# Performance work log

Hardware: AMD Instinct MI355X
Metric: run time of the kernel (lower is better)

Reference implementation:

```python
import jax, jax.numpy as jnp
import numpy as np

DIM = 1024
HEADS = 16
HEAD_DIM = DIM // HEADS

def setup_inputs() -> dict:
    key = jax.random.key(0)
    ks = jax.random.split(key, 5)
    x = jax.random.normal(ks[0], (4, 2048, DIM), dtype=jnp.float32)
    s = DIM ** -0.5
    W_qkv = jax.random.normal(ks[1], (DIM, 3 * DIM), dtype=jnp.float32) * s
    b_qkv = jnp.zeros((3 * DIM,), dtype=jnp.float32)
    W_proj = jax.random.normal(ks[2], (DIM, DIM), dtype=jnp.float32) * s
    b_proj = jnp.zeros((DIM,), dtype=jnp.float32)
    return {"x": x, "W_qkv": W_qkv, "b_qkv": b_qkv, "W_proj": W_proj, "b_proj": b_proj}

def reference(x, W_qkv, b_qkv, W_proj, b_proj):
    B, S, D = x.shape
    scale = HEAD_DIM ** -0.5
    qkv = x @ W_qkv + b_qkv                      # [B,S,3D]
    q, k, v = jnp.split(qkv, 3, axis=-1)         # each [B,S,D]
    def heads(t):
        return t.reshape(B, S, HEADS, HEAD_DIM).transpose(0, 2, 1, 3)  # [B,H,S,d]
    q, k, v = heads(q), heads(k), heads(v)
    attn = jnp.einsum('bhqd,bhkd->bhqk', q, k) * scale
    attn = jax.nn.softmax(attn, axis=-1)
    out = jnp.einsum('bhqk,bhkd->bhqd', attn, v)  # [B,H,S,d]
    out = out.transpose(0, 2, 1, 3).reshape(B, S, D)
    return out @ W_proj + b_proj
```

## Files before the change

kernel.cpp:

```cpp
#include <hip/hip_runtime.h>
#include <hip/hip_bf16.h>
#include <cstdint>


#define SEQ   2048
#define NDIM  1024
#define HEADS 16
#define HD    64

typedef __attribute__((ext_vector_type(8))) short bf16x8;
typedef __attribute__((ext_vector_type(4))) float f32x4;

typedef __attribute__((address_space(1))) void glob_void;
typedef __attribute__((address_space(3))) void lds_void;

__device__ __forceinline__ float b2f(short s) {
    return __uint_as_float(((uint32_t)(uint16_t)s) << 16);
}
__device__ __forceinline__ short f2b(float f) {
    uint32_t u = __float_as_uint(f);
    u += 0x7FFF + ((u >> 16) & 1);
    return (short)(u >> 16);
}
__device__ __forceinline__ uint32_t pk2(float a, float b) {
    return (uint32_t)(uint16_t)f2b(a) | ((uint32_t)(uint16_t)f2b(b) << 16);
}

__global__ __launch_bounds__(256) void sentinel_k(float* __restrict__ out, float v, int n) {
    const int i = blockIdx.x * 256 + threadIdx.x;
    if (i < n) out[i] = v;
}

__global__ __launch_bounds__(256) void transpose_k(const float* __restrict__ W,
                                                   short* __restrict__ WT,
                                                   int R, int C) {
    __shared__ short t[32][33];
    const int bx = blockIdx.x * 32;
    const int by = blockIdx.y * 32;
    const int tx = threadIdx.x, ty = threadIdx.y;
#pragma unroll
    for (int i = 0; i < 32; i += 8)
        t[ty + i][tx] = f2b(W[(size_t)(by + ty + i) * C + bx + tx]);
    __syncthreads();
#pragma unroll
    for (int i = 0; i < 32; i += 8)
        WT[(size_t)(bx + ty + i) * R + by + tx] = t[tx][ty + i];
}

__global__ __launch_bounds__(256) void gemm_bt(const void* __restrict__ A,
                                               const short* __restrict__ BT,
                                               const float* __restrict__ bias,
                                               void* __restrict__ Cout,
                                               int N, int K, int lda,
                                               int amode, int cmode) {
    __shared__ short As[128 * 64];
    __shared__ short Bs[128 * 64];

    const short* Ab = (const short*)A;
    const float* Af = (const float*)A;

    const int tid  = threadIdx.x;
    const int lane = tid & 63;
    const int wid  = tid >> 6;
    const int ln16 = lane & 15;
    const int quad = lane >> 4;
    const int wm = (wid & 1) * 64;
    const int wn = (wid >> 1) * 64;
    const int bm = blockIdx.y * 128;
    const int bn = blockIdx.x * 128;

    f32x4 acc[4][4];
#pragma unroll
    for (int i = 0; i < 4; ++i)
#pragma unroll
        for (int j = 0; j < 4; ++j) {
            acc[i][j][0] = 0.f; acc[i][j][1] = 0.f; acc[i][j][2] = 0.f; acc[i][j][3] = 0.f;
        }

    const int rbase = tid >> 3;
    const int k8    = (tid & 7) * 8;

    for (int ks = 0; ks < K; ks += 64) {
        __syncthreads();
#pragma unroll
        for (int i = 0; i < 4; ++i) {
            const int row = i * 32 + rbase;
            const int c   = i * 256 + tid;
            const short* gb = BT + (size_t)(bn + row) * K + ks + k8;
            __builtin_amdgcn_global_load_lds((glob_void*)gb, (lds_void*)(Bs + c * 8), 16, 0, 0);
        }
        if (amode) {
#pragma unroll
            for (int i = 0; i < 4; ++i) {
                const int row = i * 32 + rbase;
                const int c   = i * 256 + tid;
                const short* ga = Ab + (size_t)(bm + row) * lda + ks + k8;
                __builtin_amdgcn_global_load_lds((glob_void*)ga, (lds_void*)(As + c * 8), 16, 0, 0);
            }
        } else {
#pragma unroll
            for (int i = 0; i < 4; ++i) {
                const int row = i * 32 + rbase;
                const int c   = i * 256 + tid;
                const float* ga = Af + (size_t)(bm + row) * lda + ks + k8;
                const float4 f0 = *(const float4*)ga;
                const float4 f1 = *(const float4*)(ga + 4);
                union { bf16x8 v; short s[8]; } u;
                u.s[0] = f2b(f0.x); u.s[1] = f2b(f0.y); u.s[2] = f2b(f0.z); u.s[3] = f2b(f0.w);
                u.s[4] = f2b(f1.x); u.s[5] = f2b(f1.y); u.s[6] = f2b(f1.z); u.s[7] = f2b(f1.w);
                *(bf16x8*)(As + c * 8) = u.v;
            }
        }
        __syncthreads();

#pragma unroll
        for (int kk = 0; kk < 2; ++kk) {
            bf16x8 a[4], b[4];
#pragma unroll
            for (int t = 0; t < 4; ++t) {
                a[t] = *(const bf16x8*)(As + (wm + t * 16 + ln16) * 64 + kk * 32 + quad * 8);
                b[t] = *(const bf16x8*)(Bs + (wn + t * 16 + ln16) * 64 + kk * 32 + quad * 8);
            }
#pragma unroll
            for (int tm = 0; tm < 4; ++tm)
#pragma unroll
                for (int tn = 0; tn < 4; ++tn)
                    acc[tm][tn] = __builtin_amdgcn_mfma_f32_16x16x32_bf16(a[tm], b[tn], acc[tm][tn], 0, 0, 0);
        }
    }

#pragma unroll
    for (int tm = 0; tm < 4; ++tm) {
        const int row = bm + wm + tm * 16 + quad * 4;
#pragma unroll
        for (int tn = 0; tn < 4; ++tn) {
            const int col = bn + wn + tn * 16 + ln16;
            const float bv = bias[col];
#pragma unroll
            for (int r = 0; r < 4; ++r) {
                const float cv = acc[tm][tn][r] + bv;
                const size_t idx = (size_t)(row + r) * N + col;
                if (cmode) ((float*)Cout)[idx] = cv;
                else       ((short*)Cout)[idx] = f2b(cv);
            }
        }
    }
}

__global__ __launch_bounds__(256, 3) void attn_k(short* qkv) {
    __shared__ __attribute__((aligned(16))) char smem[51200];
    short*    Ks   = (short*)smem;
    uint32_t* VTw  = (uint32_t*)(smem + 16384);
    short*    Ps   = (short*)(smem + 33792);
    float*    Obuf = (float*)smem;
    float*    lred = (float*)(smem + 33792);

    const int tid  = threadIdx.x;
    const int lane = tid & 63;
    const int wid  = tid >> 6;
    const int ln16 = lane & 15;
    const int quad = lane >> 4;

    const int bx = blockIdx.x;
    const int qt = bx & 31;
    const int bh = bx >> 5;
    const int b  = bh >> 4;
    const int h  = bh & 15;
    const int q0 = qt * 64;

    const size_t row0 = ((size_t)b * SEQ) * 3072 + h * HD;

#pragma unroll
    for (int i = 0; i < 2; ++i) {
        const int c = i * 256 + tid;
        __builtin_amdgcn_global_load_lds(
            (glob_void*)(qkv + row0 + (size_t)(q0 + (c >> 3)) * 3072 + (c & 7) * 8),
            (lds_void*)(Ps + c * 8), 16, 0, 0);
    }
    __syncthreads();
    bf16x8 qf[4][2];
#pragma unroll
    for (int qg = 0; qg < 4; ++qg) {
        qf[qg][0] = *(const bf16x8*)(Ps + (qg * 16 + ln16) * 64 + quad * 8);
        qf[qg][1] = *(const bf16x8*)(Ps + (qg * 16 + ln16) * 64 + 32 + quad * 8);
    }
    __syncthreads();

    float l[4] = {0.f, 0.f, 0.f, 0.f};
    f32x4 o[4][4];
#pragma unroll
    for (int t = 0; t < 4; ++t)
#pragma unroll
        for (int qg = 0; qg < 4; ++qg) {
            o[t][qg][0] = 0.f; o[t][qg][1] = 0.f; o[t][qg][2] = 0.f; o[t][qg][3] = 0.f;
        }

    const int vp   = tid & 63;
    const int vd16 = (tid >> 6) * 16;
    const int slab = wid * 32;

    for (int kb = 0; kb < SEQ; kb += 128) {
        __syncthreads();
#pragma unroll
        for (int i = 0; i < 4; ++i) {
            const int c = i * 256 + tid;
            __builtin_amdgcn_global_load_lds(
                (glob_void*)(qkv + row0 + (size_t)(kb + (c >> 3)) * 3072 + 1024 + (c & 7) * 8),
                (lds_void*)(Ks + c * 8), 16, 0, 0);
        }
        {
            const short* gv = qkv + row0 + (size_t)(kb + 2 * vp) * 3072 + 2048 + vd16;
            union { uint4 u; uint16_t s[8]; } a0, a1, b0, b1;
            a0.u = *(const uint4*)gv;
            a1.u = *(const uint4*)(gv + 8);
            b0.u = *(const uint4*)(gv + 3072);
            b1.u = *(const uint4*)(gv + 3072 + 8);
#pragma unroll
            for (int j = 0; j < 8; ++j)
                VTw[(vd16 + j) * 68 + vp] = (uint32_t)a0.s[j] | ((uint32_t)b0.s[j] << 16);
#pragma unroll
            for (int j = 0; j < 8; ++j)
                VTw[(vd16 + 8 + j) * 68 + vp] = (uint32_t)a1.s[j] | ((uint32_t)b1.s[j] << 16);
        }
        __syncthreads();

#pragma unroll
        for (int kg = 0; kg < 2; ++kg) {
            const bf16x8 a0 = *(const bf16x8*)(Ks + (slab + kg * 16 + ln16) * 64 + quad * 8);
            const bf16x8 a1 = *(const bf16x8*)(Ks + (slab + kg * 16 + ln16) * 64 + 32 + quad * 8);
#pragma unroll
            for (int qg = 0; qg < 4; ++qg) {
                f32x4 z; z[0] = 0.f; z[1] = 0.f; z[2] = 0.f; z[3] = 0.f;
                z = __builtin_amdgcn_mfma_f32_16x16x32_bf16(a0, qf[qg][0], z, 0, 0, 0);
                z = __builtin_amdgcn_mfma_f32_16x16x32_bf16(a1, qf[qg][1], z, 0, 0, 0);
                const float p0 = __expf(fmaf(z[0], 0.125f, -12.0f));
                const float p1 = __expf(fmaf(z[1], 0.125f, -12.0f));
                const float p2 = __expf(fmaf(z[2], 0.125f, -12.0f));
                const float p3 = __expf(fmaf(z[3], 0.125f, -12.0f));
                l[qg] += (p0 + p1) + (p2 + p3);
                uint32_t* pw = (uint32_t*)(Ps + (qg * 16 + ln16) * 136 + slab + kg * 16 + quad * 4);
                pw[0] = pk2(p0, p1);
                pw[1] = pk2(p2, p3);
            }
        }

        bf16x8 bp[4];
#pragma unroll
        for (int qg = 0; qg < 4; ++qg)
            bp[qg] = *(const bf16x8*)(Ps + (qg * 16 + ln16) * 136 + slab + quad * 8);
#pragma unroll
        for (int t = 0; t < 4; ++t) {
            const bf16x8 av = *(const bf16x8*)&VTw[(t * 16 + ln16) * 68 + wid * 16 + quad * 4];
#pragma unroll
            for (int qg = 0; qg < 4; ++qg)
                o[t][qg] = __builtin_amdgcn_mfma_f32_16x16x32_bf16(av, bp[qg], o[t][qg], 0, 0, 0);
        }
    }

    __syncthreads();
#pragma unroll
    for (int qg = 0; qg < 4; ++qg) {
        l[qg] += __shfl_xor(l[qg], 16, 64);
        l[qg] += __shfl_xor(l[qg], 32, 64);
    }
    if (quad == 0) {
#pragma unroll
        for (int qg = 0; qg < 4; ++qg)
            lred[wid * 64 + qg * 16 + ln16] = l[qg];
    }
    for (int w = 0; w < 4; ++w) {
        if (wid == w) {
#pragma unroll
            for (int t = 0; t < 4; ++t)
#pragma unroll
                for (int qg = 0; qg < 4; ++qg) {
                    float* dst = &Obuf[(qg * 16 + ln16) * 68 + t * 16 + quad * 4];
                    if (w == 0) {
                        *(f32x4*)dst = o[t][qg];
                    } else {
                        f32x4 prev = *(const f32x4*)dst;
                        prev[0] += o[t][qg][0]; prev[1] += o[t][qg][1];
                        prev[2] += o[t][qg][2]; prev[3] += o[t][qg][3];
                        *(f32x4*)dst = prev;
                    }
                }
        }
        __syncthreads();
    }

    const int q  = tid & 63;
    const int dc = (tid >> 6) * 16;
    const float linv = 1.0f / (lred[q] + lred[64 + q] + lred[128 + q] + lred[192 + q]);
    union { uint4 u[2]; uint32_t w[8]; } outp;
#pragma unroll
    for (int j = 0; j < 8; ++j)
        outp.w[j] = pk2(Obuf[q * 68 + dc + 2 * j] * linv, Obuf[q * 68 + dc + 2 * j + 1] * linv);
    uint4* dst = (uint4*)(qkv + row0 + (size_t)(q0 + q) * 3072 + dc);
    dst[0] = outp.u[0];
    dst[1] = outp.u[1];
}

extern "C" void kernel_launch(void* const* d_in, const int* in_sizes, int n_in,
                              void* d_out, int out_size, void* d_ws, size_t ws_size,
                              hipStream_t stream) {
    const float* x     = (const float*)d_in[0];
    const float* Wqkv  = (const float*)d_in[1];
    const float* bqkv  = (const float*)d_in[2];
    const float* Wproj = (const float*)d_in[3];
    const float* bproj = (const float*)d_in[4];
    float* out = (float*)d_out;

    int bad = -1;
    if (n_in != 5) bad = 9;
    else {
        const int want[5] = {8388608, 3145728, 3072, 1048576, 1024};
        for (int i = 0; i < 5; ++i) if (in_sizes[i] != want[i]) { bad = i; break; }
        if (bad < 0 && out_size != 8388608) bad = 8;
    }
    if (bad >= 0) {
        sentinel_k<<<(out_size + 255) / 256, 256, 0, stream>>>(out, 1000.0f + 100.0f * bad, out_size);
        return;
    }

    char* ws = (char*)d_ws;
    short* wqkvT  = (short*)(ws);
    short* wprojT = (short*)(ws + 6291456);
    short* qkv    = (short*)(ws + 8388608);

    transpose_k<<<dim3(96, 32), dim3(32, 8), 0, stream>>>(Wqkv, wqkvT, 1024, 3072);
    transpose_k<<<dim3(32, 32), dim3(32, 8), 0, stream>>>(Wproj, wprojT, 1024, 1024);

    gemm_bt<<<dim3(3072 / 128, 8192 / 128), 256, 0, stream>>>(
        x, wqkvT, bqkv, qkv, 3072, 1024, 1024, 0, 0);

    attn_k<<<dim3(4 * HEADS * (SEQ / 64)), 256, 0, stream>>>(qkv);

    gemm_bt<<<dim3(1024 / 128, 8192 / 128), 256, 0, stream>>>(
        qkv, wprojT, bproj, out, 1024, 1024, 3072, 1, 1);
}
```

Measured before the change: 353.7 us.

## Pre-convert x to bf16, load K directly to registers, use hardware bf16 pack

Adds a separate kernel that converts x to bf16 once, so the QKV GEMM can use the async global-to-LDS path for both operands instead of converting fp32 in the load loop. The attention kernel now loads K fragments straight from global memory into registers rather than staging them in LDS. This shrinks shared memory and raises the occupancy hint from 3 to 4 blocks. It also uses the hardware cvt_pk_bf16_f32 instruction for packing and writes P with a single 64-bit store. The cost is an extra kernel launch plus an x round trip through memory, and K loads are now uncoalesced per-lane global reads.

```diff
diff --git a/kernel.cpp b/kernel.cpp
--- a/kernel.cpp
+++ b/kernel.cpp
@@ -22,13 +22,33 @@
     u += 0x7FFF + ((u >> 16) & 1);
     return (short)(u >> 16);
 }
+
+#if __has_builtin(__builtin_amdgcn_cvt_pk_bf16_f32)
+typedef __attribute__((ext_vector_type(2))) __bf16 bf16x2_t;
+__device__ __forceinline__ uint32_t pk2(float a, float b) {
+    union { bf16x2_t v; uint32_t u; } c;
+    c.v = __builtin_amdgcn_cvt_pk_bf16_f32(a, b);
+    return c.u;
+}
+#else
 __device__ __forceinline__ uint32_t pk2(float a, float b) {
     return (uint32_t)(uint16_t)f2b(a) | ((uint32_t)(uint16_t)f2b(b) << 16);
 }
+#endif
 
 __global__ __launch_bounds__(256) void sentinel_k(float* __restrict__ out, float v, int n) {
     const int i = blockIdx.x * 256 + threadIdx.x;
     if (i < n) out[i] = v;
+}
+
+__global__ __launch_bounds__(256) void cvt_x_k(const float4* __restrict__ x,
+                                               uint2* __restrict__ xb) {
+    const int i = blockIdx.x * 256 + threadIdx.x;
+    const float4 f = x[i];
+    uint2 o;
+    o.x = pk2(f.x, f.y);
+    o.y = pk2(f.z, f.w);
+    xb[i] = o;
 }
 
 __global__ __launch_bounds__(256) void transpose_k(const float* __restrict__ W,
@@ -47,17 +67,13 @@
         WT[(size_t)(bx + ty + i) * R + by + tx] = t[tx][ty + i];
 }
 
-__global__ __launch_bounds__(256) void gemm_bt(const void* __restrict__ A,
+__global__ __launch_bounds__(256) void gemm_bt(const short* __restrict__ A,
                                                const short* __restrict__ BT,
                                                const float* __restrict__ bias,
                                                void* __restrict__ Cout,
-                                               int N, int K, int lda,
-                                               int amode, int cmode) {
+                                               int N, int K, int lda, int cmode) {
     __shared__ short As[128 * 64];
     __shared__ short Bs[128 * 64];
-
-    const short* Ab = (const short*)A;
-    const float* Af = (const float*)A;
 
     const int tid  = threadIdx.x;
     const int lane = tid & 63;
@@ -87,29 +103,9 @@
             const int row = i * 32 + rbase;
             const int c   = i * 256 + tid;
             const short* gb = BT + (size_t)(bn + row) * K + ks + k8;
+            const short* ga = A  + (size_t)(bm + row) * lda + ks + k8;
             __builtin_amdgcn_global_load_lds((glob_void*)gb, (lds_void*)(Bs + c * 8), 16, 0, 0);
-        }
-        if (amode) {
-#pragma unroll
-            for (int i = 0; i < 4; ++i) {
-                const int row = i * 32 + rbase;
-                const int c   = i * 256 + tid;
-                const short* ga = Ab + (size_t)(bm + row) * lda + ks + k8;
-                __builtin_amdgcn_global_load_lds((glob_void*)ga, (lds_void*)(As + c * 8), 16, 0, 0);
-            }
-        } else {
-#pragma unroll
-            for (int i = 0; i < 4; ++i) {
-                const int row = i * 32 + rbase;
-                const int c   = i * 256 + tid;
-                const float* ga = Af + (size_t)(bm + row) * lda + ks + k8;
-                const float4 f0 = *(const float4*)ga;
-                const float4 f1 = *(const float4*)(ga + 4);
-                union { bf16x8 v; short s[8]; } u;
-                u.s[0] = f2b(f0.x); u.s[1] = f2b(f0.y); u.s[2] = f2b(f0.z); u.s[3] = f2b(f0.w);
-                u.s[4] = f2b(f1.x); u.s[5] = f2b(f1.y); u.s[6] = f2b(f1.z); u.s[7] = f2b(f1.w);
-                *(bf16x8*)(As + c * 8) = u.v;
-            }
+            __builtin_amdgcn_global_load_lds((glob_void*)ga, (lds_void*)(As + c * 8), 16, 0, 0);
         }
         __syncthreads();
 
@@ -147,13 +143,12 @@
     }
 }
 
-__global__ __launch_bounds__(256, 3) void attn_k(short* qkv) {
-    __shared__ __attribute__((aligned(16))) char smem[51200];
-    short*    Ks   = (short*)smem;
-    uint32_t* VTw  = (uint32_t*)(smem + 16384);
-    short*    Ps   = (short*)(smem + 33792);
+__global__ __launch_bounds__(256, 4) void attn_k(short* qkv) {
+    __shared__ __attribute__((aligned(16))) char smem[34816];
+    uint32_t* VTw  = (uint32_t*)smem;
+    short*    Ps   = (short*)(smem + 17408);
     float*    Obuf = (float*)smem;
-    float*    lred = (float*)(smem + 33792);
+    float*    lred = (float*)(smem + 17408);
 
     const int tid  = threadIdx.x;
     const int lane = tid & 63;
@@ -199,15 +194,17 @@
     const int vd16 = (tid >> 6) * 16;
     const int slab = wid * 32;
 
+    const short* kbase = qkv + row0 + (size_t)(slab + ln16) * 3072 + 1024 + quad * 8;
+
     for (int kb = 0; kb < SEQ; kb += 128) {
-        __syncthreads();
-#pragma unroll
-        for (int i = 0; i < 4; ++i) {
-            const int c = i * 256 + tid;
-            __builtin_amdgcn_global_load_lds(
-                (glob_void*)(qkv + row0 + (size_t)(kb + (c >> 3)) * 3072 + 1024 + (c & 7) * 8),
-                (lds_void*)(Ks + c * 8), 16, 0, 0);
-        }
+        bf16x8 kf[2][2];
+#pragma unroll
+        for (int kg = 0; kg < 2; ++kg) {
+            const short* gk = kbase + (size_t)(kb + kg * 16) * 3072;
+            kf[kg][0] = *(const bf16x8*)gk;
+            kf[kg][1] = *(const bf16x8*)(gk + 32);
+        }
+        __syncthreads();
         {
             const short* gv = qkv + row0 + (size_t)(kb + 2 * vp) * 3072 + 2048 + vd16;
             union { uint4 u; uint16_t s[8]; } a0, a1, b0, b1;
@@ -226,21 +223,18 @@
 
 #pragma unroll
         for (int kg = 0; kg < 2; ++kg) {
-            const bf16x8 a0 = *(const bf16x8*)(Ks + (slab + kg * 16 + ln16) * 64 + quad * 8);
-            const bf16x8 a1 = *(const bf16x8*)(Ks + (slab + kg * 16 + ln16) * 64 + 32 + quad * 8);
 #pragma unroll
             for (int qg = 0; qg < 4; ++qg) {
                 f32x4 z; z[0] = 0.f; z[1] = 0.f; z[2] = 0.f; z[3] = 0.f;
-                z = __builtin_amdgcn_mfma_f32_16x16x32_bf16(a0, qf[qg][0], z, 0, 0, 0);
-                z = __builtin_amdgcn_mfma_f32_16x16x32_bf16(a1, qf[qg][1], z, 0, 0, 0);
+                z = __builtin_amdgcn_mfma_f32_16x16x32_bf16(kf[kg][0], qf[qg][0], z, 0, 0, 0);
+                z = __builtin_amdgcn_mfma_f32_16x16x32_bf16(kf[kg][1], qf[qg][1], z, 0, 0, 0);
                 const float p0 = __expf(fmaf(z[0], 0.125f, -12.0f));
                 const float p1 = __expf(fmaf(z[1], 0.125f, -12.0f));
                 const float p2 = __expf(fmaf(z[2], 0.125f, -12.0f));
                 const float p3 = __expf(fmaf(z[3], 0.125f, -12.0f));
                 l[qg] += (p0 + p1) + (p2 + p3);
-                uint32_t* pw = (uint32_t*)(Ps + (qg * 16 + ln16) * 136 + slab + kg * 16 + quad * 4);
-                pw[0] = pk2(p0, p1);
-                pw[1] = pk2(p2, p3);
+                uint2 pw; pw.x = pk2(p0, p1); pw.y = pk2(p2, p3);
+                *(uint2*)(Ps + (qg * 16 + ln16) * 136 + slab + kg * 16 + quad * 4) = pw;
             }
         }
 
@@ -326,15 +320,17 @@
     short* wqkvT  = (short*)(ws);
     short* wprojT = (short*)(ws + 6291456);
     short* qkv    = (short*)(ws + 8388608);
-
+    short* xb     = (short*)(ws + 58720256);
+
+    cvt_x_k<<<8192, 256, 0, stream>>>((const float4*)x, (uint2*)xb);
     transpose_k<<<dim3(96, 32), dim3(32, 8), 0, stream>>>(Wqkv, wqkvT, 1024, 3072);
     transpose_k<<<dim3(32, 32), dim3(32, 8), 0, stream>>>(Wproj, wprojT, 1024, 1024);
 
     gemm_bt<<<dim3(3072 / 128, 8192 / 128), 256, 0, stream>>>(
-        x, wqkvT, bqkv, qkv, 3072, 1024, 1024, 0, 0);
+        xb, wqkvT, bqkv, qkv, 3072, 1024, 1024, 0);
 
     attn_k<<<dim3(4 * HEADS * (SEQ / 64)), 256, 0, stream>>>(qkv);
 
     gemm_bt<<<dim3(1024 / 128, 8192 / 128), 256, 0, stream>>>(
-        qkv, wprojT, bproj, out, 1024, 1024, 3072, 1, 1);
-}
+        qkv, wprojT, bproj, out, 1024, 1024, 3072, 1);
+}
```

Measured after the change: 721.3 us. 104% more time.
